# Kernel tuning notes

Hardware: AMD Instinct MI355X
Metric: run time of the kernel (lower is better)

The kernel has to match this reference:

```python
import jax, jax.numpy as jnp
import numpy as np

B, S, R = 8, 4096, 512
E, K, ATOMS, XAR, TOPK = 64, 256, 16, 3, 2
TEMP = 1.0


def setup_inputs() -> dict:
    key = jax.random.key(0)
    k0, k1, k2, k3, k4 = jax.random.split(key, 5)
    x_latent = jax.random.normal(k0, (B, S, R), jnp.float32)
    router_w = jax.random.normal(k1, (E, R), jnp.float32) * (1.0 / np.sqrt(R))
    atoms = jax.random.normal(k2, (E, ATOMS, R), jnp.float32) * 0.01
    combo_weights = jax.random.uniform(k3, (E, K, XAR), jnp.float32) * 0.5 + 0.25
    combo_logits = jax.random.normal(k4, (E, K, XAR, ATOMS), jnp.float32) * 0.01
    return {"x_latent": x_latent, "router_w": router_w, "atoms": atoms,
            "combo_weights": combo_weights, "combo_logits": combo_logits}


def _expert_centroids(atoms, combo_weights, combo_logits):
    # Hard codeword path (vectorized over experts):
    # sign atoms -> pick argmax atom per (k, xor slot) -> weight -> sum -> sign -> mean over k
    binary = jnp.sign(atoms)                                   # [E, A, R]
    # softmax(logits/t) then argmax == argmax(logits) (monotone)
    idx = jnp.argmax(combo_logits, axis=-1)                    # [E, K, XAR]
    sel = binary[jnp.arange(E)[:, None, None], idx]            # [E, K, XAR, R]
    codewords = jnp.sign((sel * combo_weights[..., None]).sum(axis=2))  # [E, K, R]
    return codewords.mean(axis=1)                              # [E, R]


def reference(x_latent, router_w, atoms, combo_weights, combo_logits):
    t = max(TEMP, 0.1)
    router_logits = jnp.einsum('bsr,er->bse', x_latent, router_w)   # [B, S, E]
    probs_t = jax.nn.softmax(router_logits / t, axis=-1)
    gates, expert_ids = jax.lax.top_k(probs_t, TOPK)                # [B, S, 2]
    gates = gates / gates.sum(axis=-1, keepdims=True)

    centroids = _expert_centroids(atoms, combo_weights, combo_logits)  # [E, R]

    # aux load-balancing loss (uses untempered softmax)
    router_prob = jax.nn.softmax(router_logits, axis=-1)
    aux_loss = E * jnp.sum(router_prob.mean(axis=(0, 1)) *
                           (router_prob > 0).astype(x_latent.dtype).mean(axis=(0, 1)))

    # dense per-expert gate = sum over topk slots of gate * (id == e), then combine with centroids
    dense_gates = (jax.nn.one_hot(expert_ids, E, dtype=gates.dtype) *
                   gates[..., None]).sum(axis=-2)                    # [B, S, E]
    combined = jnp.einsum('bse,er->bsr', dense_gates, centroids)     # [B, S, R]
    return combined, aux_loss
```

## Files before the change

kernel.cpp:

```cpp
#include <hip/hip_runtime.h>
#include <math.h>

#define TOKENS 32768
#define RDIM 512
#define NEXP 64
#define NK 256
#define LDB 264
#define PSTR 67
#define TAU 4.0e-3f

typedef unsigned short u16;
typedef float f32x4 __attribute__((ext_vector_type(4)));
typedef short s16x8 __attribute__((ext_vector_type(8)));

#define MFMA_B16(a, b, c) __builtin_amdgcn_mfma_f32_16x16x32_bf16(a, b, c, 0, 0, 0)

__device__ __forceinline__ void split_pack(float4 v, unsigned& h01, unsigned& h23,
                                           unsigned& l01, unsigned& l23) {
    unsigned u0 = __float_as_uint(v.x), u1 = __float_as_uint(v.y);
    unsigned u2 = __float_as_uint(v.z), u3 = __float_as_uint(v.w);
    float r0 = v.x - __uint_as_float(u0 & 0xFFFF0000u);
    float r1 = v.y - __uint_as_float(u1 & 0xFFFF0000u);
    float r2 = v.z - __uint_as_float(u2 & 0xFFFF0000u);
    float r3 = v.w - __uint_as_float(u3 & 0xFFFF0000u);
    h01 = (u0 >> 16) | (u1 & 0xFFFF0000u);
    h23 = (u2 >> 16) | (u3 & 0xFFFF0000u);
    l01 = (__float_as_uint(r0) >> 16) | (__float_as_uint(r1) & 0xFFFF0000u);
    l23 = (__float_as_uint(r2) >> 16) | (__float_as_uint(r3) & 0xFFFF0000u);
}

__device__ __forceinline__ void split8(float4 a, float4 b, s16x8& hi, s16x8& lo) {
    union U { unsigned u[4]; s16x8 v; };
    U H, L;
    split_pack(a, H.u[0], H.u[1], L.u[0], L.u[1]);
    split_pack(b, H.u[2], H.u[3], L.u[2], L.u[3]);
    hi = H.v; lo = L.v;
}

__global__ __launch_bounds__(256) void centroid_kernel(
    const float* __restrict__ atoms,
    const float* __restrict__ cw,
    const float* __restrict__ cl,
    float* __restrict__ cent,
    float* __restrict__ aux_sum,
    unsigned* __restrict__ aux_cnt)
{
    __shared__ unsigned pack[NK];
    const int e    = blockIdx.x >> 1;
    const int half = blockIdx.x & 1;
    const int tid  = threadIdx.x;

    if (blockIdx.x == 0 && tid < 64) { aux_sum[tid] = 0.f; aux_cnt[tid] = 0u; }

    {
        const int k = tid;
        unsigned u = 0;
        float w3[3];
        #pragma unroll
        for (int xx = 0; xx < 3; ++xx) {
            const float* cp = cl + ((((size_t)e * NK + k) * 3 + xx) << 4);
            float v[16];
            *(float4*)(v + 0)  = *(const float4*)(cp + 0);
            *(float4*)(v + 4)  = *(const float4*)(cp + 4);
            *(float4*)(v + 8)  = *(const float4*)(cp + 8);
            *(float4*)(v + 12) = *(const float4*)(cp + 12);
            float best = v[0]; int bi = 0;
            #pragma unroll
            for (int a = 1; a < 16; ++a) {
                if (v[a] > best) { best = v[a]; bi = a; }
            }
            u |= (unsigned)bi << (4 * xx);
            w3[xx] = cw[((size_t)e * NK + k) * 3 + xx];
        }
        unsigned lut = 0;
        #pragma unroll
        for (int c = 0; c < 8; ++c) {
            float val = ((c & 1) ? -w3[0] : w3[0])
                      + ((c & 2) ? -w3[1] : w3[1])
                      + ((c & 4) ? -w3[2] : w3[2]);
            lut |= (val < 0.f ? 1u : 0u) << c;
        }
        pack[k] = u | (lut << 16);
    }

    const int r = half * 256 + tid;
    unsigned B0 = 0;
    #pragma unroll
    for (int a = 0; a < 16; ++a)
        B0 |= (atoms[((size_t)e * 16 + a) * RDIM + r] < 0.f ? 1u : 0u) << a;
    __syncthreads();

    int n0 = 0;
    for (int k = 0; k < NK; ++k) {
        unsigned u  = pack[k];
        unsigned i0 = u & 15u, i1 = (u >> 4) & 15u, i2 = (u >> 8) & 15u;
        unsigned c0 = ((B0 >> i0) & 1u) | (((B0 >> i1) & 1u) << 1) | (((B0 >> i2) & 1u) << 2);
        n0 += (u >> (16 + c0)) & 1u;
    }
    cent[(size_t)e * RDIM + r] = 1.f - (float)n0 * (1.f / 128.f);
}

__global__ __launch_bounds__(512, 4) void moe_main(
    const float* __restrict__ x,
    const float* __restrict__ w,
    const float* __restrict__ cent,
    float* __restrict__ out,
    float* __restrict__ aux_sum,
    unsigned* __restrict__ aux_cnt)
{
    __shared__ u16 wlds[2 * 64 * LDB];
    u16* whi = wlds;
    u16* wlo = wlds + 64 * LDB;
    float* P     = (float*)wlds;
    float* candv = P + 64 * PSTR;
    int*   candi = (int*)(candv + 64 * 25);
    float* qsum  = (float*)(candi + 64 * 25);
    float* gateL = qsum + 64 * 9;
    __shared__ float s_aux[64];
    __shared__ unsigned s_cnt[64];

    const int tid  = threadIdx.x;
    const int lane = tid & 63;
    const int wave = tid >> 6;
    const int l15  = lane & 15;
    const int kgrp = (lane >> 4) << 3;
    const int tok0 = blockIdx.x * 64;
    const int tokG = wave >> 1;
    const int expG = wave & 1;

    if (tid < 64) { s_aux[tid] = 0.f; s_cnt[tid] = 0u; }

    f32x4 acc[2];
    acc[0] = (f32x4){0.f,0.f,0.f,0.f};
    acc[1] = (f32x4){0.f,0.f,0.f,0.f};

    const float* xlane = x + (size_t)(tok0 + tokG * 16 + l15) * RDIM + kgrp;
    const int wrow = tid >> 3;
    const int wseg = tid & 7;
    const float* wg = w + (size_t)wrow * RDIM + wseg * 32;
    const int woff = wrow * LDB + wseg * 32;

    for (int h = 0; h < 2; ++h) {
        const float* xb = xlane + h * 256;
        float4 p0a = *(const float4*)(xb);      float4 p0b = *(const float4*)(xb + 4);
        float4 p1a = *(const float4*)(xb + 32); float4 p1b = *(const float4*)(xb + 36);
        float4 p2a = *(const float4*)(xb + 64); float4 p2b = *(const float4*)(xb + 68);

        __syncthreads();
        #pragma unroll
        for (int j = 0; j < 8; ++j) {
            float4 wv = *(const float4*)(wg + h * 256 + j * 4);
            unsigned h01, h23, l01, l23;
            split_pack(wv, h01, h23, l01, l23);
            *(uint2*)&whi[woff + j * 4] = make_uint2(h01, h23);
            *(uint2*)&wlo[woff + j * 4] = make_uint2(l01, l23);
        }
        __syncthreads();

        #pragma unroll
        for (int kb = 0; kb < 8; ++kb) {
            s16x8 ah, al;
            split8(p0a, p0b, ah, al);
            p0a = p1a; p0b = p1b; p1a = p2a; p1b = p2b;
            if (kb < 5) {
                const float* nx = xb + (kb + 3) * 32;
                p2a = *(const float4*)(nx);
                p2b = *(const float4*)(nx + 4);
            }
            const int kl = kb * 32 + kgrp;
            #pragma unroll
            for (int nt = 0; nt < 2; ++nt) {
                const int brow = expG * 32 + nt * 16 + l15;
                s16x8 bh = *(const s16x8*)&whi[brow * LDB + kl];
                s16x8 bl = *(const s16x8*)&wlo[brow * LDB + kl];
                acc[nt] = MFMA_B16(ah, bh, acc[nt]);
                acc[nt] = MFMA_B16(ah, bl, acc[nt]);
                acc[nt] = MFMA_B16(al, bh, acc[nt]);
            }
        }
    }

    __syncthreads();
    #pragma unroll
    for (int nt = 0; nt < 2; ++nt)
        #pragma unroll
        for (int i = 0; i < 4; ++i)
            P[(tokG * 16 + ((lane >> 4) << 2) + i) * PSTR + expG * 32 + nt * 16 + l15] = acc[nt][i];
    __syncthreads();

    const int tt = tid & 63;
    const int ss = tid >> 6;
    float v[8];
    #pragma unroll
    for (int j = 0; j < 8; ++j) v[j] = P[tt * PSTR + ss * 8 + j];

    float m1 = -INFINITY, m2 = -INFINITY, m3 = -INFINITY;
    int   i1 = NEXP, i2 = NEXP, i3 = NEXP;
    #pragma unroll
    for (int j = 0; j < 8; ++j) {
        float val = v[j]; int e = ss * 8 + j;
        if (val > m1)      { m3 = m2; i3 = i2; m2 = m1; i2 = i1; m1 = val; i1 = e; }
        else if (val > m2) { m3 = m2; i3 = i2; m2 = val; i2 = e; }
        else if (val > m3) { m3 = val; i3 = e; }
    }
    candv[tt * 25 + ss * 3 + 0] = m1; candi[tt * 25 + ss * 3 + 0] = i1;
    candv[tt * 25 + ss * 3 + 1] = m2; candi[tt * 25 + ss * 3 + 1] = i2;
    candv[tt * 25 + ss * 3 + 2] = m3; candi[tt * 25 + ss * 3 + 2] = i3;
    __syncthreads();

    m1 = m2 = m3 = -INFINITY; i1 = i2 = i3 = NEXP;
    #pragma unroll
    for (int q = 0; q < 24; ++q) {
        float val = candv[tt * 25 + q]; int e = candi[tt * 25 + q];
        if (val > m1)      { m3 = m2; i3 = i2; m2 = m1; i2 = i1; m1 = val; i1 = e; }
        else if (val > m2) { m3 = m2; i3 = i2; m2 = val; i2 = e; }
        else if (val > m3) { m3 = val; i3 = e; }
    }

    float ex[8]; float ps = 0.f;
    #pragma unroll
    for (int j = 0; j < 8; ++j) { ex[j] = __expf(v[j] - m1); ps += ex[j]; }
    qsum[tt * 9 + ss] = ps;

    if (ss == 0) {
        {
            const float ed  = __expf(m2 - m1);
            const float inv = 1.f / (1.f + ed);
            gateL[tt * 4 + 0] = inv;
            gateL[tt * 4 + 1] = ed * inv;
            ((int*)gateL)[tt * 4 + 2] = i1;
            ((int*)gateL)[tt * 4 + 3] = i2;
        }
        unsigned long long bmask = __ballot(m2 - m3 < TAU);
        while (bmask) {
            const int f = __ffsll(bmask) - 1;
            bmask &= bmask - 1;
            int id3[3];
            id3[0] = __shfl(i1, f); id3[1] = __shfl(i2, f); id3[2] = __shfl(i3, f);
            const float* xrow = x + (size_t)(tok0 + f) * RDIM + lane * 8;
            float4 a0 = *(const float4*)(xrow);
            float4 a1 = *(const float4*)(xrow + 4);
            float d[3];
            #pragma unroll
            for (int jj = 0; jj < 3; ++jj) {
                const float* wrow = w + (size_t)id3[jj] * RDIM + lane * 8;
                float4 b0 = *(const float4*)(wrow);
                float4 b1 = *(const float4*)(wrow + 4);
                float p = a0.x * b0.x;
                p = fmaf(a0.y, b0.y, p); p = fmaf(a0.z, b0.z, p); p = fmaf(a0.w, b0.w, p);
                p = fmaf(a1.x, b1.x, p); p = fmaf(a1.y, b1.y, p);
                p = fmaf(a1.z, b1.z, p); p = fmaf(a1.w, b1.w, p);
                #pragma unroll
                for (int off = 32; off; off >>= 1) p += __shfl_xor(p, off);
                d[jj] = p;
            }
            int b = 0;
            if (d[1] > d[0] || (d[1] == d[0] && id3[1] < id3[0])) b = 1;
            if (d[2] > d[b] || (d[2] == d[b] && id3[2] < id3[b])) b = 2;
            int sec;
            if (b == 0)      sec = (d[1] > d[2] || (d[1] == d[2] && id3[1] < id3[2])) ? 1 : 2;
            else if (b == 1) sec = (d[0] > d[2] || (d[0] == d[2] && id3[0] < id3[2])) ? 0 : 2;
            else             sec = (d[0] > d[1] || (d[0] == d[1] && id3[0] < id3[1])) ? 0 : 1;
            if (lane == f) {
                const float ed  = __expf(d[sec] - d[b]);
                const float inv = 1.f / (1.f + ed);
                gateL[f * 4 + 0] = inv;
                gateL[f * 4 + 1] = ed * inv;
                ((int*)gateL)[f * 4 + 2] = id3[b];
                ((int*)gateL)[f * 4 + 3] = id3[sec];
            }
        }
    }
    __syncthreads();

    float Z = 0.f;
    #pragma unroll
    for (int k = 0; k < 8; ++k) Z += qsum[tt * 9 + k];
    const float invZ = 1.f / Z;
    #pragma unroll
    for (int j = 0; j < 8; ++j) P[tt * PSTR + ss * 8 + j] = ex[j] * invZ;
    __syncthreads();

    {
        const int e = tid & 63, tq = tid >> 6;
        float s = 0.f; unsigned cn = 0u;
        #pragma unroll
        for (int t = 0; t < 8; ++t) {
            float pv = P[(tq * 8 + t) * PSTR + e];
            s += pv; cn += (pv > 0.f) ? 1u : 0u;
        }
        atomicAdd(&s_aux[e], s);
        atomicAdd(&s_cnt[e], cn);
    }
    __syncthreads();
    if (tid < 64) {
        atomicAdd(aux_sum + tid, s_aux[tid]);
        atomicAdd(aux_cnt + tid, s_cnt[tid]);
    }

    {
        const int e = lane;
        #pragma unroll
        for (int s2 = 0; s2 < 8; ++s2) {
            const int t2 = wave * 8 + s2;
            float4 g4 = *(float4*)&gateL[t2 * 4];
            const float g1 = g4.x, g2 = g4.y;
            const int e1 = __float_as_int(g4.z), e2 = __float_as_int(g4.w);
            const float4* c1 = (const float4*)(cent + (size_t)e1 * RDIM);
            const float4* c2 = (const float4*)(cent + (size_t)e2 * RDIM);
            float4* op = (float4*)(out + (size_t)(tok0 + t2) * RDIM);
            float4 A0 = c1[e],      Bb0 = c2[e];
            float4 A1 = c1[e + 64], Bb1 = c2[e + 64];
            float4 o0, o1;
            o0.x = fmaf(g1, A0.x, g2 * Bb0.x); o0.y = fmaf(g1, A0.y, g2 * Bb0.y);
            o0.z = fmaf(g1, A0.z, g2 * Bb0.z); o0.w = fmaf(g1, A0.w, g2 * Bb0.w);
            o1.x = fmaf(g1, A1.x, g2 * Bb1.x); o1.y = fmaf(g1, A1.y, g2 * Bb1.y);
            o1.z = fmaf(g1, A1.z, g2 * Bb1.z); o1.w = fmaf(g1, A1.w, g2 * Bb1.w);
            op[e]      = o0;
            op[e + 64] = o1;
        }
    }
}

__global__ __launch_bounds__(64) void aux_kernel(
    const float* __restrict__ sums,
    const unsigned* __restrict__ cnts,
    float* __restrict__ out_aux)
{
    const int e = threadIdx.x;
    float v = (sums[e] * (1.f / (float)TOKENS)) * ((float)cnts[e] * (1.f / (float)TOKENS));
    #pragma unroll
    for (int off = 32; off; off >>= 1) v += __shfl_xor(v, off);
    if (e == 0) out_aux[0] = (float)NEXP * v;
}

extern "C" void kernel_launch(void* const* d_in, const int* in_sizes, int n_in,
                              void* d_out, int out_size, void* d_ws, size_t ws_size,
                              hipStream_t stream) {
    const float* x     = (const float*)d_in[0];
    const float* rw    = (const float*)d_in[1];
    const float* atoms = (const float*)d_in[2];
    const float* cwts  = (const float*)d_in[3];
    const float* clog  = (const float*)d_in[4];
    float* out = (float*)d_out;

    float*    aux_sum = (float*)d_ws;
    unsigned* aux_cnt = (unsigned*)((char*)d_ws + 256);
    float*    cent    = (float*)((char*)d_ws + 512);

    centroid_kernel<<<128, 256, 0, stream>>>(atoms, cwts, clog, cent, aux_sum, aux_cnt);
    moe_main<<<512, 512, 0, stream>>>(x, rw, cent, out, aux_sum, aux_cnt);
    aux_kernel<<<1, 64, 0, stream>>>(aux_sum, aux_cnt, out + (size_t)TOKENS * RDIM);
}
```

Before: 162.2 us.

## Double tokens per block, prefetch router weights, fuse aux reduction via last-block counter

Each block now handles 128 tokens instead of 64. Every wave computes all 64 experts for its 16 tokens, so the split router weights staged in LDS are reused across twice as many tokens and half as many blocks repeat the staging. Weight and x loads are prefetched into registers ahead of use, and the first-half barrier is dropped. When the workspace is large enough, the final aux-loss reduction runs in the last block to finish, tracked by an atomic done counter, which saves a separate kernel launch. The cost is more registers (launch bounds drop to 2 blocks per CU) and only 256 blocks, which may underfill the GPU.

```diff
diff --git a/kernel.cpp b/kernel.cpp
--- a/kernel.cpp
+++ b/kernel.cpp
@@ -43,7 +43,8 @@
     const float* __restrict__ cl,
     float* __restrict__ cent,
     float* __restrict__ aux_sum,
-    unsigned* __restrict__ aux_cnt)
+    unsigned* __restrict__ aux_cnt,
+    unsigned* __restrict__ done)
 {
     __shared__ unsigned pack[NK];
     const int e    = blockIdx.x >> 1;
@@ -51,6 +52,7 @@
     const int tid  = threadIdx.x;
 
     if (blockIdx.x == 0 && tid < 64) { aux_sum[tid] = 0.f; aux_cnt[tid] = 0u; }
+    if (done && blockIdx.x == 0 && tid == 0) *done = 0u;
 
     {
         const int k = tid;
@@ -100,58 +102,66 @@
     cent[(size_t)e * RDIM + r] = 1.f - (float)n0 * (1.f / 128.f);
 }
 
-__global__ __launch_bounds__(512, 4) void moe_main(
+__global__ __launch_bounds__(512, 2) void moe_main(
     const float* __restrict__ x,
     const float* __restrict__ w,
     const float* __restrict__ cent,
     float* __restrict__ out,
     float* __restrict__ aux_sum,
-    unsigned* __restrict__ aux_cnt)
+    unsigned* __restrict__ aux_cnt,
+    unsigned* __restrict__ done,
+    float* __restrict__ out_aux,
+    int fuse)
 {
     __shared__ u16 wlds[2 * 64 * LDB];
     u16* whi = wlds;
     u16* wlo = wlds + 64 * LDB;
     float* P     = (float*)wlds;
-    float* candv = P + 64 * PSTR;
-    int*   candi = (int*)(candv + 64 * 25);
-    float* qsum  = (float*)(candi + 64 * 25);
-    float* gateL = qsum + 64 * 9;
+    float* candv = P + 128 * PSTR;
+    int*   candi = (int*)(candv + 128 * 13);
+    float* qsum  = (float*)(candi + 128 * 13);
+    float* gateL = qsum + 128 * 5;
     __shared__ float s_aux[64];
     __shared__ unsigned s_cnt[64];
+    __shared__ int s_last;
 
     const int tid  = threadIdx.x;
     const int lane = tid & 63;
     const int wave = tid >> 6;
     const int l15  = lane & 15;
     const int kgrp = (lane >> 4) << 3;
-    const int tok0 = blockIdx.x * 64;
-    const int tokG = wave >> 1;
-    const int expG = wave & 1;
+    const int tok0 = blockIdx.x * 128;
 
     if (tid < 64) { s_aux[tid] = 0.f; s_cnt[tid] = 0u; }
 
-    f32x4 acc[2];
-    acc[0] = (f32x4){0.f,0.f,0.f,0.f};
-    acc[1] = (f32x4){0.f,0.f,0.f,0.f};
-
-    const float* xlane = x + (size_t)(tok0 + tokG * 16 + l15) * RDIM + kgrp;
+    f32x4 acc[4];
+    #pragma unroll
+    for (int nt = 0; nt < 4; ++nt) acc[nt] = (f32x4){0.f, 0.f, 0.f, 0.f};
+
+    const float* xlane = x + (size_t)(tok0 + wave * 16 + l15) * RDIM + kgrp;
     const int wrow = tid >> 3;
     const int wseg = tid & 7;
     const float* wg = w + (size_t)wrow * RDIM + wseg * 32;
     const int woff = wrow * LDB + wseg * 32;
 
+    float4 wpre[8];
+    #pragma unroll
+    for (int j = 0; j < 8; ++j) wpre[j] = *(const float4*)(wg + j * 4);
+
+    float4 preA[4], preB[4];
+    #pragma unroll
+    for (int i = 0; i < 4; ++i) {
+        preA[i] = *(const float4*)(xlane + i * 32);
+        preB[i] = *(const float4*)(xlane + i * 32 + 4);
+    }
+
+    #pragma unroll
     for (int h = 0; h < 2; ++h) {
-        const float* xb = xlane + h * 256;
-        float4 p0a = *(const float4*)(xb);      float4 p0b = *(const float4*)(xb + 4);
-        float4 p1a = *(const float4*)(xb + 32); float4 p1b = *(const float4*)(xb + 36);
-        float4 p2a = *(const float4*)(xb + 64); float4 p2b = *(const float4*)(xb + 68);
-
-        __syncthreads();
+        if (h) __syncthreads();
         #pragma unroll
         for (int j = 0; j < 8; ++j) {
-            float4 wv = *(const float4*)(wg + h * 256 + j * 4);
             unsigned h01, h23, l01, l23;
-            split_pack(wv, h01, h23, l01, l23);
+            split_pack(wpre[j], h01, h23, l01, l23);
             *(uint2*)&whi[woff + j * 4] = make_uint2(h01, h23);
             *(uint2*)&wlo[woff + j * 4] = make_uint2(l01, l23);
         }
@@ -160,17 +170,22 @@
         #pragma unroll
         for (int kb = 0; kb < 8; ++kb) {
             s16x8 ah, al;
-            split8(p0a, p0b, ah, al);
-            p0a = p1a; p0b = p1b; p1a = p2a; p1b = p2b;
-            if (kb < 5) {
-                const float* nx = xb + (kb + 3) * 32;
-                p2a = *(const float4*)(nx);
-                p2b = *(const float4*)(nx + 4);
+            split8(preA[kb & 3], preB[kb & 3], ah, al);
+            const int gk = h * 8 + kb + 4;
+            if (gk < 16) {
+                const float* nx = xlane + gk * 32;
+                preA[kb & 3] = *(const float4*)(nx);
+                preB[kb & 3] = *(const float4*)(nx + 4);
+            }
+            if (h == 0 && kb == 2) {
+                #pragma unroll
+                for (int j = 0; j < 8; ++j)
+                    wpre[j] = *(const float4*)(wg + 256 + j * 4);
             }
             const int kl = kb * 32 + kgrp;
             #pragma unroll
-            for (int nt = 0; nt < 2; ++nt) {
-                const int brow = expG * 32 + nt * 16 + l15;
+            for (int nt = 0; nt < 4; ++nt) {
+                const int brow = nt * 16 + l15;
                 s16x8 bh = *(const s16x8*)&whi[brow * LDB + kl];
                 s16x8 bl = *(const s16x8*)&wlo[brow * LDB + kl];
                 acc[nt] = MFMA_B16(ah, bh, acc[nt]);
@@ -182,45 +197,45 @@
 
     __syncthreads();
     #pragma unroll
-    for (int nt = 0; nt < 2; ++nt)
+    for (int nt = 0; nt < 4; ++nt)
         #pragma unroll
         for (int i = 0; i < 4; ++i)
-            P[(tokG * 16 + ((lane >> 4) << 2) + i) * PSTR + expG * 32 + nt * 16 + l15] = acc[nt][i];
-    __syncthreads();
-
-    const int tt = tid & 63;
-    const int ss = tid >> 6;
-    float v[8];
-    #pragma unroll
-    for (int j = 0; j < 8; ++j) v[j] = P[tt * PSTR + ss * 8 + j];
+            P[(wave * 16 + ((lane >> 4) << 2) + i) * PSTR + nt * 16 + l15] = acc[nt][i];
+    __syncthreads();
+
+    const int tt = tid & 127;
+    const int ss = tid >> 7;
+    float v[16];
+    #pragma unroll
+    for (int j = 0; j < 16; ++j) v[j] = P[tt * PSTR + ss * 16 + j];
 
     float m1 = -INFINITY, m2 = -INFINITY, m3 = -INFINITY;
     int   i1 = NEXP, i2 = NEXP, i3 = NEXP;
     #pragma unroll
-    for (int j = 0; j < 8; ++j) {
-        float val = v[j]; int e = ss * 8 + j;
+    for (int j = 0; j < 16; ++j) {
+        float val = v[j]; int e = ss * 16 + j;
         if (val > m1)      { m3 = m2; i3 = i2; m2 = m1; i2 = i1; m1 = val; i1 = e; }
         else if (val > m2) { m3 = m2; i3 = i2; m2 = val; i2 = e; }
         else if (val > m3) { m3 = val; i3 = e; }
     }
-    candv[tt * 25 + ss * 3 + 0] = m1; candi[tt * 25 + ss * 3 + 0] = i1;
-    candv[tt * 25 + ss * 3 + 1] = m2; candi[tt * 25 + ss * 3 + 1] = i2;
-    candv[tt * 25 + ss * 3 + 2] = m3; candi[tt * 25 + ss * 3 + 2] = i3;
+    candv[tt * 13 + ss * 3 + 0] = m1; candi[tt * 13 + ss * 3 + 0] = i1;
+    candv[tt * 13 + ss * 3 + 1] = m2; candi[tt * 13 + ss * 3 + 1] = i2;
+    candv[tt * 13 + ss * 3 + 2] = m3; candi[tt * 13 + ss * 3 + 2] = i3;
     __syncthreads();
 
     m1 = m2 = m3 = -INFINITY; i1 = i2 = i3 = NEXP;
     #pragma unroll
-    for (int q = 0; q < 24; ++q) {
-        float val = candv[tt * 25 + q]; int e = candi[tt * 25 + q];
+    for (int q = 0; q < 12; ++q) {
+        float val = candv[tt * 13 + q]; int e = candi[tt * 13 + q];
         if (val > m1)      { m3 = m2; i3 = i2; m2 = m1; i2 = i1; m1 = val; i1 = e; }
         else if (val > m2) { m3 = m2; i3 = i2; m2 = val; i2 = e; }
         else if (val > m3) { m3 = val; i3 = e; }
     }
 
-    float ex[8]; float ps = 0.f;
-    #pragma unroll
-    for (int j = 0; j < 8; ++j) { ex[j] = __expf(v[j] - m1); ps += ex[j]; }
-    qsum[tt * 9 + ss] = ps;
+    float ex[16]; float ps = 0.f;
+    #pragma unroll
+    for (int j = 0; j < 16; ++j) { ex[j] = __expf(v[j] - m1); ps += ex[j]; }
+    qsum[tt * 5 + ss] = ps;
 
     if (ss == 0) {
         {
@@ -231,13 +246,14 @@
             ((int*)gateL)[tt * 4 + 2] = i1;
             ((int*)gateL)[tt * 4 + 3] = i2;
         }
+        const int tbase = wave << 6;
         unsigned long long bmask = __ballot(m2 - m3 < TAU);
         while (bmask) {
             const int f = __ffsll(bmask) - 1;
             bmask &= bmask - 1;
             int id3[3];
             id3[0] = __shfl(i1, f); id3[1] = __shfl(i2, f); id3[2] = __shfl(i3, f);
-            const float* xrow = x + (size_t)(tok0 + f) * RDIM + lane * 8;
+            const float* xrow = x + (size_t)(tok0 + tbase + f) * RDIM + lane * 8;
             float4 a0 = *(const float4*)(xrow);
             float4 a1 = *(const float4*)(xrow + 4);
             float d[3];
@@ -264,10 +280,10 @@
             if (lane == f) {
                 const float ed  = __expf(d[sec] - d[b]);
                 const float inv = 1.f / (1.f + ed);
-                gateL[f * 4 + 0] = inv;
-                gateL[f * 4 + 1] = ed * inv;
-                ((int*)gateL)[f * 4 + 2] = id3[b];
-                ((int*)gateL)[f * 4 + 3] = id3[sec];
+                gateL[(tbase + f) * 4 + 0] = inv;
+                gateL[(tbase + f) * 4 + 1] = ed * inv;
+                ((int*)gateL)[(tbase + f) * 4 + 2] = id3[b];
+                ((int*)gateL)[(tbase + f) * 4 + 3] = id3[sec];
             }
         }
     }
@@ -275,18 +291,18 @@
 
     float Z = 0.f;
     #pragma unroll
-    for (int k = 0; k < 8; ++k) Z += qsum[tt * 9 + k];
+    for (int k = 0; k < 4; ++k) Z += qsum[tt * 5 + k];
     const float invZ = 1.f / Z;
     #pragma unroll
-    for (int j = 0; j < 8; ++j) P[tt * PSTR + ss * 8 + j] = ex[j] * invZ;
+    for (int j = 0; j < 16; ++j) P[tt * PSTR + ss * 16 + j] = ex[j] * invZ;
     __syncthreads();
 
     {
         const int e = tid & 63, tq = tid >> 6;
         float s = 0.f; unsigned cn = 0u;
         #pragma unroll
-        for (int t = 0; t < 8; ++t) {
-            float pv = P[(tq * 8 + t) * PSTR + e];
+        for (int t = 0; t < 16; ++t) {
+            float pv = P[(tq * 16 + t) * PSTR + e];
             s += pv; cn += (pv > 0.f) ? 1u : 0u;
         }
         atomicAdd(&s_aux[e], s);
@@ -301,8 +317,8 @@
     {
         const int e = lane;
         #pragma unroll
-        for (int s2 = 0; s2 < 8; ++s2) {
-            const int t2 = wave * 8 + s2;
+        for (int s2 = 0; s2 < 16; ++s2) {
+            const int t2 = wave * 16 + s2;
             float4 g4 = *(float4*)&gateL[t2 * 4];
             const float g1 = g4.x, g2 = g4.y;
             const int e1 = __float_as_int(g4.z), e2 = __float_as_int(g4.w);
@@ -320,6 +336,23 @@
             op[e + 64] = o1;
         }
     }
+
+    if (fuse) {
+        __syncthreads();
+        if (tid == 0) {
+            __threadfence();
+            s_last = (atomicAdd(done, 1u) == 255u) ? 1 : 0;
+        }
+        __syncthreads();
+        if (s_last && tid < 64) {
+            float    sv = atomicAdd(&aux_sum[tid], 0.f);
+            unsigned cv = atomicAdd(&aux_cnt[tid], 0u);
+            float val = (sv * (1.f / (float)TOKENS)) * ((float)cv * (1.f / (float)TOKENS));
+            #pragma unroll
+            for (int off = 32; off; off >>= 1) val += __shfl_xor(val, off);
+            if (tid == 0) out_aux[0] = (float)NEXP * val;
+        }
+    }
 }
 
 __global__ __launch_bounds__(64) void aux_kernel(
@@ -344,11 +377,15 @@
     const float* clog  = (const float*)d_in[4];
     float* out = (float*)d_out;
 
+    const bool fused = ws_size >= (size_t)(1024 + NEXP * RDIM * 4);
     float*    aux_sum = (float*)d_ws;
     unsigned* aux_cnt = (unsigned*)((char*)d_ws + 256);
-    float*    cent    = (float*)((char*)d_ws + 512);
-
-    centroid_kernel<<<128, 256, 0, stream>>>(atoms, cwts, clog, cent, aux_sum, aux_cnt);
-    moe_main<<<512, 512, 0, stream>>>(x, rw, cent, out, aux_sum, aux_cnt);
-    aux_kernel<<<1, 64, 0, stream>>>(aux_sum, aux_cnt, out + (size_t)TOKENS * RDIM);
-}
+    unsigned* done    = fused ? (unsigned*)((char*)d_ws + 512) : nullptr;
+    float*    cent    = (float*)((char*)d_ws + (fused ? 1024 : 512));
+
+    centroid_kernel<<<128, 256, 0, stream>>>(atoms, cwts, clog, cent, aux_sum, aux_cnt, done);
+    moe_main<<<256, 512, 0, stream>>>(x, rw, cent, out, aux_sum, aux_cnt, done,
+                                      out + (size_t)TOKENS * RDIM, fused ? 1 : 0);
+    if (!fused)
+        aux_kernel<<<1, 64, 0, stream>>>(aux_sum, aux_cnt, out + (size_t)TOKENS * RDIM);
+}
```

New measurement: 163.0 us. About the same (+0.5%).

## Fuse centroid and aux kernels into main MoE kernel via ticket scheduling

Applied to the files above, without the earlier changes.

Folds the centroid computation into the main kernel: the first 128 blocks, ordered by an atomic ticket, each compute one centroid slice and bump a release flag. All blocks spin on that flag before the output combine, and the last block to finish computes the aux loss, so two launches are replaced by one kernel plus a memset. The main GEMM loop also prefetches the router weights for both halves into registers and uses a four-deep rotating x prefetch, which removes one barrier. The spin-wait relies on the ticket blocks running before others depend on them, and the extra prefetch registers may pressure occupancy.

```diff
diff --git a/kernel.cpp b/kernel.cpp
--- a/kernel.cpp
+++ b/kernel.cpp
@@ -37,22 +37,12 @@
     hi = H.v; lo = L.v;
 }
 
-__global__ __launch_bounds__(256) void centroid_kernel(
-    const float* __restrict__ atoms,
-    const float* __restrict__ cw,
-    const float* __restrict__ cl,
-    float* __restrict__ cent,
-    float* __restrict__ aux_sum,
-    unsigned* __restrict__ aux_cnt)
+__device__ __forceinline__ void centroid_slice(
+    int e, int half, int tid,
+    const float* __restrict__ atoms, const float* __restrict__ cw,
+    const float* __restrict__ cl, float* __restrict__ cent, unsigned* pack)
 {
-    __shared__ unsigned pack[NK];
-    const int e    = blockIdx.x >> 1;
-    const int half = blockIdx.x & 1;
-    const int tid  = threadIdx.x;
-
-    if (blockIdx.x == 0 && tid < 64) { aux_sum[tid] = 0.f; aux_cnt[tid] = 0u; }
-
-    {
+    if (tid < 256) {
         const int k = tid;
         unsigned u = 0;
         float w3[3];
@@ -82,31 +72,57 @@
         }
         pack[k] = u | (lut << 16);
     }
-
-    const int r = half * 256 + tid;
-    unsigned B0 = 0;
-    #pragma unroll
-    for (int a = 0; a < 16; ++a)
-        B0 |= (atoms[((size_t)e * 16 + a) * RDIM + r] < 0.f ? 1u : 0u) << a;
-    __syncthreads();
-
-    int n0 = 0;
-    for (int k = 0; k < NK; ++k) {
-        unsigned u  = pack[k];
-        unsigned i0 = u & 15u, i1 = (u >> 4) & 15u, i2 = (u >> 8) & 15u;
-        unsigned c0 = ((B0 >> i0) & 1u) | (((B0 >> i1) & 1u) << 1) | (((B0 >> i2) & 1u) << 2);
-        n0 += (u >> (16 + c0)) & 1u;
-    }
-    cent[(size_t)e * RDIM + r] = 1.f - (float)n0 * (1.f / 128.f);
-}
-
-__global__ __launch_bounds__(512, 4) void moe_main(
+    __syncthreads();
+    if (tid < 256) {
+        const int r = half * 256 + tid;
+        unsigned B0 = 0;
+        #pragma unroll
+        for (int a = 0; a < 16; ++a)
+            B0 |= (atoms[((size_t)e * 16 + a) * RDIM + r] < 0.f ? 1u : 0u) << a;
+        int n0 = 0;
+        #pragma unroll 2
+        for (int k = 0; k < NK; k += 8) {
+            unsigned pk[8];
+            #pragma unroll
+            for (int j = 0; j < 8; ++j) pk[j] = pack[k + j];
+            #pragma unroll
+            for (int j = 0; j < 8; ++j) {
+                unsigned u  = pk[j];
+                unsigned i0 = u & 15u, i1 = (u >> 4) & 15u, i2 = (u >> 8) & 15u;
+                unsigned c0 = ((B0 >> i0) & 1u) | (((B0 >> i1) & 1u) << 1) | (((B0 >> i2) & 1u) << 2);
+                n0 += (u >> (16 + c0)) & 1u;
+            }
+        }
+        cent[(size_t)e * RDIM + r] = 1.f - (float)n0 * (1.f / 128.f);
+    }
+    __syncthreads();
+}
+
+__global__ __launch_bounds__(256) void centroid_kernel(
+    const float* __restrict__ atoms,
+    const float* __restrict__ cw,
+    const float* __restrict__ cl,
+    float* __restrict__ cent)
+{
+    __shared__ unsigned pack[NK];
+    centroid_slice(blockIdx.x >> 1, blockIdx.x & 1, threadIdx.x, atoms, cw, cl, cent, pack);
+}
+
+__global__ __launch_bounds__(512, 4) void moe_fused(
     const float* __restrict__ x,
     const float* __restrict__ w,
-    const float* __restrict__ cent,
+    const float* __restrict__ atoms,
+    const float* __restrict__ cw,
+    const float* __restrict__ cl,
+    float* __restrict__ cent,
     float* __restrict__ out,
     float* __restrict__ aux_sum,
-    unsigned* __restrict__ aux_cnt)
+    unsigned* __restrict__ aux_cnt,
+    unsigned* __restrict__ ticket,
+    unsigned* __restrict__ cflag,
+    unsigned* __restrict__ done,
+    float* __restrict__ out_aux,
+    int fuse)
 {
     __shared__ u16 wlds[2 * 64 * LDB];
     u16* whi = wlds;
@@ -118,6 +134,8 @@
     float* gateL = qsum + 64 * 9;
     __shared__ float s_aux[64];
     __shared__ unsigned s_cnt[64];
+    __shared__ unsigned s_my;
+    __shared__ int s_last;
 
     const int tid  = threadIdx.x;
     const int lane = tid & 63;
@@ -129,6 +147,15 @@
     const int expG = wave & 1;
 
     if (tid < 64) { s_aux[tid] = 0.f; s_cnt[tid] = 0u; }
+    if (fuse && tid == 0) s_my = atomicAdd(ticket, 1u);
+    __syncthreads();
+
+    if (fuse && s_my < 128u) {
+        centroid_slice((int)(s_my >> 1), (int)(s_my & 1u), tid, atoms, cw, cl, cent,
+                       (unsigned*)wlds);
+        if (tid == 0)
+            __hip_atomic_fetch_add(cflag, 1u, __ATOMIC_RELEASE, __HIP_MEMORY_SCOPE_AGENT);
+    }
 
     f32x4 acc[2];
     acc[0] = (f32x4){0.f,0.f,0.f,0.f};
@@ -140,18 +167,26 @@
     const float* wg = w + (size_t)wrow * RDIM + wseg * 32;
     const int woff = wrow * LDB + wseg * 32;
 
+    float4 wpre[8];
+    #pragma unroll
+    for (int j = 0; j < 8; ++j) wpre[j] = *(const float4*)(wg + j * 4);
+
+    float4 preA[4], preB[4];
+    #pragma unroll
+    for (int i = 0; i < 4; ++i) {
+        preA[i] = *(const float4*)(xlane + i * 32);
+        preB[i] = *(const float4*)(xlane + i * 32 + 4);
+    }
+
+    const int arow = tokG * 16 + l15;
+
+    #pragma unroll
     for (int h = 0; h < 2; ++h) {
-        const float* xb = xlane + h * 256;
-        float4 p0a = *(const float4*)(xb);      float4 p0b = *(const float4*)(xb + 4);
-        float4 p1a = *(const float4*)(xb + 32); float4 p1b = *(const float4*)(xb + 36);
-        float4 p2a = *(const float4*)(xb + 64); float4 p2b = *(const float4*)(xb + 68);
-
-        __syncthreads();
+        if (h) __syncthreads();
         #pragma unroll
         for (int j = 0; j < 8; ++j) {
-            float4 wv = *(const float4*)(wg + h * 256 + j * 4);
             unsigned h01, h23, l01, l23;
-            split_pack(wv, h01, h23, l01, l23);
+            split_pack(wpre[j], h01, h23, l01, l23);
             *(uint2*)&whi[woff + j * 4] = make_uint2(h01, h23);
             *(uint2*)&wlo[woff + j * 4] = make_uint2(l01, l23);
         }
@@ -160,12 +195,17 @@
         #pragma unroll
         for (int kb = 0; kb < 8; ++kb) {
             s16x8 ah, al;
-            split8(p0a, p0b, ah, al);
-            p0a = p1a; p0b = p1b; p1a = p2a; p1b = p2b;
-            if (kb < 5) {
-                const float* nx = xb + (kb + 3) * 32;
-                p2a = *(const float4*)(nx);
-                p2b = *(const float4*)(nx + 4);
+            split8(preA[kb & 3], preB[kb & 3], ah, al);
+            const int gk = h * 8 + kb + 4;
+            if (gk < 16) {
+                const float* nx = xlane + gk * 32;
+                preA[kb & 3] = *(const float4*)(nx);
+                preB[kb & 3] = *(const float4*)(nx + 4);
+            }
+            if (h == 0 && kb == 2) {
+                #pragma unroll
+                for (int j = 0; j < 8; ++j)
+                    wpre[j] = *(const float4*)(wg + 256 + j * 4);
             }
             const int kl = kb * 32 + kgrp;
             #pragma unroll
@@ -296,6 +336,14 @@
     if (tid < 64) {
         atomicAdd(aux_sum + tid, s_aux[tid]);
         atomicAdd(aux_cnt + tid, s_cnt[tid]);
+    }
+
+    if (fuse) {
+        if (tid == 0) {
+            while (__hip_atomic_load(cflag, __ATOMIC_ACQUIRE, __HIP_MEMORY_SCOPE_AGENT) < 128u)
+                __builtin_amdgcn_s_sleep(8);
+        }
+        __syncthreads();
     }
 
     {
@@ -320,6 +368,23 @@
             op[e + 64] = o1;
         }
     }
+
+    if (fuse) {
+        __syncthreads();
+        if (tid == 0) {
+            __threadfence();
+            s_last = (atomicAdd(done, 1u) == 511u) ? 1 : 0;
+        }
+        __syncthreads();
+        if (s_last && tid < 64) {
+            float    sv = atomicAdd(&aux_sum[tid], 0.f);
+            unsigned cv = atomicAdd(&aux_cnt[tid], 0u);
+            float val = (sv * (1.f / (float)TOKENS)) * ((float)cv * (1.f / (float)TOKENS));
+            #pragma unroll
+            for (int off = 32; off; off >>= 1) val += __shfl_xor(val, off);
+            if (tid == 0) out_aux[0] = (float)NEXP * val;
+        }
+    }
 }
 
 __global__ __launch_bounds__(64) void aux_kernel(
@@ -343,12 +408,27 @@
     const float* cwts  = (const float*)d_in[3];
     const float* clog  = (const float*)d_in[4];
     float* out = (float*)d_out;
-
+    float* out_aux = out + (size_t)TOKENS * RDIM;
+
+    const bool fused = ws_size >= (size_t)(1024 + NEXP * RDIM * 4);
     float*    aux_sum = (float*)d_ws;
     unsigned* aux_cnt = (unsigned*)((char*)d_ws + 256);
-    float*    cent    = (float*)((char*)d_ws + 512);
-
-    centroid_kernel<<<128, 256, 0, stream>>>(atoms, cwts, clog, cent, aux_sum, aux_cnt);
-    moe_main<<<512, 512, 0, stream>>>(x, rw, cent, out, aux_sum, aux_cnt);
-    aux_kernel<<<1, 64, 0, stream>>>(aux_sum, aux_cnt, out + (size_t)TOKENS * RDIM);
-}
+    unsigned* ticket  = (unsigned*)((char*)d_ws + 512);
+    unsigned* cflag   = (unsigned*)((char*)d_ws + 516);
+    unsigned* done    = (unsigned*)((char*)d_ws + 520);
+    float*    cent    = (float*)((char*)d_ws + (fused ? 1024 : 512));
+
+    if (fused) {
+        hipMemsetAsync(d_ws, 0, 1024, stream);
+        moe_fused<<<512, 512, 0, stream>>>(x, rw, atoms, cwts, clog, cent, out,
+                                           aux_sum, aux_cnt, ticket, cflag, done,
+                                           out_aux, 1);
+    } else {
+        hipMemsetAsync(d_ws, 0, 512, stream);
+        centroid_kernel<<<128, 256, 0, stream>>>(atoms, cwts, clog, cent);
+        moe_fused<<<512, 512, 0, stream>>>(x, rw, atoms, cwts, clog, cent, out,
+                                           aux_sum, aux_cnt, nullptr, nullptr, nullptr,
+                                           out_aux, 0);
+        aux_kernel<<<1, 64, 0, stream>>>(aux_sum, aux_cnt, out_aux);
+    }
+}
```

Result: slower. 189.0 us (+16.5%).
